# Optimization experiments

Measured on AMD Instinct MI355X. Metric: run time of the kernel, lower is better.

## Reference

```python
import jax, jax.numpy as jnp
import numpy as np

SIGMA = 1.2
SIGMA_SQ = jnp.float32(SIGMA * SIGMA)


def setup_inputs() -> dict:
    key = jax.random.key(0)
    k1, k2, k3 = jax.random.split(key, 3)
    X = jax.random.normal(k1, (32768, 2), dtype=jnp.float32)
    pattern_layer = jax.random.normal(k2, (8192, 2), dtype=jnp.float32)
    W2 = jax.random.normal(k3, (8192,), dtype=jnp.float32)
    return {"X": X, "pattern_layer": pattern_layer, "W2": W2}


def reference(X, pattern_layer, W2):
    # Pairwise squared distances via |a|^2 + |b|^2 - 2 a.b  -> [N, P]
    x_sq = jnp.sum(X * X, axis=1, keepdims=True)              # [N, 1]
    p_sq = jnp.sum(pattern_layer * pattern_layer, axis=1)     # [P]
    cross = X @ pattern_layer.T                               # [N, P]
    Dsq = x_sq + p_sq[None, :] - 2.0 * cross                  # [N, P]
    K = jnp.exp(-Dsq / (2.0 * SIGMA_SQ))                      # RBF kernel [N, P]
    num = K @ W2                                              # [N]
    den = jnp.sum(K, axis=1)                                  # [N]
    return num / den
```

## Files before the change

kernel.cpp:

```cpp
#include <hip/hip_runtime.h>

#define N 32768
#define P 8192
#define SLICES 8
#define XPB 64
#define PATS_PER_SLICE (P / SLICES)

#define RBF_F 0.50093577808645257f

static __device__ __forceinline__ float fast_exp2(float x) {
#if __has_builtin(__builtin_amdgcn_exp2f)
    return __builtin_amdgcn_exp2f(x);
#else
    return exp2f(x);
#endif
}

__global__ void prep_kernel(const float* __restrict__ pat,
                            const float* __restrict__ w2,
                            float4* __restrict__ c) {
    int i = blockIdx.x * blockDim.x + threadIdx.x;
    if (i < P) {
        float p0 = pat[2 * i];
        float p1 = pat[2 * i + 1];
        float4 v;
        v.x = 2.0f * RBF_F * p0;
        v.y = 2.0f * RBF_F * p1;
        v.z = -RBF_F * (p0 * p0 + p1 * p1);
        v.w = w2[i];
        c[i] = v;
    }
}

__global__ __launch_bounds__(SLICES * XPB) void
rbf_kernel(const float* __restrict__ X,
           const float4* __restrict__ c,
           float* __restrict__ out) {
    const int t  = threadIdx.x;
    const int xl = t & (XPB - 1);
    const int xi = blockIdx.x * XPB + xl;
    const int slice = __builtin_amdgcn_readfirstlane(t >> 6);

    const float2 xv = ((const float2*)X)[xi];
    const float x0 = xv.x, x1 = xv.y;

    const float4* __restrict__ cp = c + slice * PATS_PER_SLICE;

    float n0 = 0.f, n1 = 0.f, n2 = 0.f, n3 = 0.f;
    float d0 = 0.f, d1 = 0.f, d2 = 0.f, d3 = 0.f;

#pragma unroll 4
    for (int j = 0; j < PATS_PER_SLICE; j += 4) {
        float4 a = cp[j + 0];
        float4 b = cp[j + 1];
        float4 e = cp[j + 2];
        float4 g = cp[j + 3];

        float k0 = fast_exp2(fmaf(a.y, x1, fmaf(a.x, x0, a.z)));
        float k1 = fast_exp2(fmaf(b.y, x1, fmaf(b.x, x0, b.z)));
        float k2 = fast_exp2(fmaf(e.y, x1, fmaf(e.x, x0, e.z)));
        float k3 = fast_exp2(fmaf(g.y, x1, fmaf(g.x, x0, g.z)));

        d0 += k0; n0 = fmaf(k0, a.w, n0);
        d1 += k1; n1 = fmaf(k1, b.w, n1);
        d2 += k2; n2 = fmaf(k2, e.w, n2);
        d3 += k3; n3 = fmaf(k3, g.w, n3);
    }

    float num = (n0 + n1) + (n2 + n3);
    float den = (d0 + d1) + (d2 + d3);

    __shared__ float snum[SLICES][XPB];
    __shared__ float sden[SLICES][XPB];
    snum[slice][xl] = num;
    sden[slice][xl] = den;
    __syncthreads();

    if (t < XPB) {
        float nn = 0.f, dd = 0.f;
#pragma unroll
        for (int s = 0; s < SLICES; ++s) {
            nn += snum[s][t];
            dd += sden[s][t];
        }
        out[blockIdx.x * XPB + t] = nn / dd;
    }
}

extern "C" void kernel_launch(void* const* d_in, const int* in_sizes, int n_in,
                              void* d_out, int out_size, void* d_ws, size_t ws_size,
                              hipStream_t stream) {
    const float* X   = (const float*)d_in[0];
    const float* pat = (const float*)d_in[1];
    const float* w2  = (const float*)d_in[2];
    float* out = (float*)d_out;
    float4* c = (float4*)d_ws;

    prep_kernel<<<(P + 255) / 256, 256, 0, stream>>>(pat, w2, c);
    rbf_kernel<<<N / XPB, SLICES * XPB, 0, stream>>>(X, c, out);
}
```

Before: 109.2 us.

## Repack pattern constants into pair layout and use packed FP32 FMA

The prep kernel now stores patterns in pairs laid out structure-of-arrays within two float4s, so the main loop can evaluate two patterns at once with packed 2-wide FMA (v_pk_fma_f32) for both the exponent argument and the weighted accumulation. This cuts the VALU instruction count per pattern, leaving the transcendental exp2 as the main per-pattern cost. Slices per block double to 16 (1024 threads), which halves the per-thread loop length but doubles the shared-memory reduction and block size and may limit occupancy.

```diff
diff --git a/kernel.cpp b/kernel.cpp
--- a/kernel.cpp
+++ b/kernel.cpp
@@ -2,11 +2,14 @@
 
 #define N 32768
 #define P 8192
-#define SLICES 8
+#define SLICES 16
 #define XPB 64
 #define PATS_PER_SLICE (P / SLICES)
+#define PAIRS_PER_SLICE (PATS_PER_SLICE / 2)
 
 #define RBF_F 0.50093577808645257f
+
+typedef float v2f __attribute__((ext_vector_type(2)));
 
 static __device__ __forceinline__ float fast_exp2(float x) {
 #if __has_builtin(__builtin_amdgcn_exp2f)
@@ -19,16 +22,18 @@
 __global__ void prep_kernel(const float* __restrict__ pat,
                             const float* __restrict__ w2,
                             float4* __restrict__ c) {
-    int i = blockIdx.x * blockDim.x + threadIdx.x;
-    if (i < P) {
-        float p0 = pat[2 * i];
-        float p1 = pat[2 * i + 1];
-        float4 v;
-        v.x = 2.0f * RBF_F * p0;
-        v.y = 2.0f * RBF_F * p1;
-        v.z = -RBF_F * (p0 * p0 + p1 * p1);
-        v.w = w2[i];
-        c[i] = v;
+    int q = blockIdx.x * blockDim.x + threadIdx.x;
+    if (q < P / 2) {
+        float p00 = pat[4 * q + 0], p01 = pat[4 * q + 1];
+        float p10 = pat[4 * q + 2], p11 = pat[4 * q + 3];
+        float4 a, b;
+        a.x = 2.0f * RBF_F * p00;  a.y = 2.0f * RBF_F * p10;
+        a.z = 2.0f * RBF_F * p01;  a.w = 2.0f * RBF_F * p11;
+        b.x = -RBF_F * (p00 * p00 + p01 * p01);
+        b.y = -RBF_F * (p10 * p10 + p11 * p11);
+        b.z = w2[2 * q];           b.w = w2[2 * q + 1];
+        c[2 * q]     = a;
+        c[2 * q + 1] = b;
     }
 }
 
@@ -42,33 +47,41 @@
     const int slice = __builtin_amdgcn_readfirstlane(t >> 6);
 
     const float2 xv = ((const float2*)X)[xi];
-    const float x0 = xv.x, x1 = xv.y;
+    const v2f x0v = { xv.x, xv.x };
+    const v2f x1v = { xv.y, xv.y };
 
-    const float4* __restrict__ cp = c + slice * PATS_PER_SLICE;
+    const float4* __restrict__ cp = c + (size_t)slice * (2 * PAIRS_PER_SLICE);
 
-    float n0 = 0.f, n1 = 0.f, n2 = 0.f, n3 = 0.f;
-    float d0 = 0.f, d1 = 0.f, d2 = 0.f, d3 = 0.f;
+    v2f n0 = {0.f, 0.f}, n1 = {0.f, 0.f};
+    v2f d0 = {0.f, 0.f}, d1 = {0.f, 0.f};
 
-#pragma unroll 4
-    for (int j = 0; j < PATS_PER_SLICE; j += 4) {
-        float4 a = cp[j + 0];
-        float4 b = cp[j + 1];
-        float4 e = cp[j + 2];
-        float4 g = cp[j + 3];
+#pragma unroll 2
+    for (int q = 0; q < PAIRS_PER_SLICE; q += 2) {
+        float4 a0 = cp[2 * q + 0];
+        float4 a1 = cp[2 * q + 1];
+        float4 b0 = cp[2 * q + 2];
+        float4 b1 = cp[2 * q + 3];
 
-        float k0 = fast_exp2(fmaf(a.y, x1, fmaf(a.x, x0, a.z)));
-        float k1 = fast_exp2(fmaf(b.y, x1, fmaf(b.x, x0, b.z)));
-        float k2 = fast_exp2(fmaf(e.y, x1, fmaf(e.x, x0, e.z)));
-        float k3 = fast_exp2(fmaf(g.y, x1, fmaf(g.x, x0, g.z)));
+        v2f ta = __builtin_elementwise_fma((v2f){a0.x, a0.y}, x0v,
+                                           (v2f){a1.x, a1.y});
+        ta = __builtin_elementwise_fma((v2f){a0.z, a0.w}, x1v, ta);
+        v2f tb = __builtin_elementwise_fma((v2f){b0.x, b0.y}, x0v,
+                                           (v2f){b1.x, b1.y});
+        tb = __builtin_elementwise_fma((v2f){b0.z, b0.w}, x1v, tb);
 
-        d0 += k0; n0 = fmaf(k0, a.w, n0);
-        d1 += k1; n1 = fmaf(k1, b.w, n1);
-        d2 += k2; n2 = fmaf(k2, e.w, n2);
-        d3 += k3; n3 = fmaf(k3, g.w, n3);
+        v2f ka = { fast_exp2(ta.x), fast_exp2(ta.y) };
+        v2f kb = { fast_exp2(tb.x), fast_exp2(tb.y) };
+
+        d0 += ka;
+        n0 = __builtin_elementwise_fma(ka, (v2f){a1.z, a1.w}, n0);
+        d1 += kb;
+        n1 = __builtin_elementwise_fma(kb, (v2f){b1.z, b1.w}, n1);
     }
 
-    float num = (n0 + n1) + (n2 + n3);
-    float den = (d0 + d1) + (d2 + d3);
+    v2f nv = n0 + n1;
+    v2f dv = d0 + d1;
+    float num = nv.x + nv.y;
+    float den = dv.x + dv.y;
 
     __shared__ float snum[SLICES][XPB];
     __shared__ float sden[SLICES][XPB];
@@ -96,6 +109,6 @@
     float* out = (float*)d_out;
     float4* c = (float4*)d_ws;
 
-    prep_kernel<<<(P + 255) / 256, 256, 0, stream>>>(pat, w2, c);
+    prep_kernel<<<(P / 2 + 255) / 256, 256, 0, stream>>>(pat, w2, c);
     rbf_kernel<<<N / XPB, SLICES * XPB, 0, stream>>>(X, c, out);
 }
```

Result: faster. 99.15 us (-9.2%).

## Stage pattern tiles in LDS via async loads and use packed FMA over multiple points

Applied to the files above, without the earlier changes.

Swaps the mapping: each lane now handles a pattern and each wave covers 8 X points, where before each thread walked the patterns for a single point. Pattern tiles are double-buffered into LDS with global_load_lds, and the math uses packed v2f FMAs. Results are reduced with cross-lane shuffles and then shared memory. The intent is to cut per-thread global/L2 loads of the pattern constants and raise ALU throughput with packed ops, but exp2 throughput stays the bound. The change also adds a shuffle reduction and a sync per tile.

```diff
diff --git a/kernel.cpp b/kernel.cpp
--- a/kernel.cpp
+++ b/kernel.cpp
@@ -2,11 +2,20 @@
 
 #define N 32768
 #define P 8192
-#define SLICES 8
-#define XPB 64
-#define PATS_PER_SLICE (P / SLICES)
+#define TILE 1024
+#define NTILES (P / TILE)
+#define XG 4
+#define MX 8
+#define XPB (XG * MX)
+#define THREADS 512
+#define NBLK (N / XPB)
 
 #define RBF_F 0.50093577808645257f
+
+typedef float v2f __attribute__((ext_vector_type(2)));
+
+#define AS1 __attribute__((address_space(1)))
+#define AS3 __attribute__((address_space(3)))
 
 static __device__ __forceinline__ float fast_exp2(float x) {
 #if __has_builtin(__builtin_amdgcn_exp2f)
@@ -32,57 +41,97 @@
     }
 }
 
-__global__ __launch_bounds__(SLICES * XPB) void
+__global__ __launch_bounds__(THREADS, 8) void
 rbf_kernel(const float* __restrict__ X,
            const float4* __restrict__ c,
            float* __restrict__ out) {
-    const int t  = threadIdx.x;
-    const int xl = t & (XPB - 1);
-    const int xi = blockIdx.x * XPB + xl;
-    const int slice = __builtin_amdgcn_readfirstlane(t >> 6);
+    __shared__ float4 buf[2][TILE];
+    __shared__ float red[XG][2][MX][2];
 
-    const float2 xv = ((const float2*)X)[xi];
-    const float x0 = xv.x, x1 = xv.y;
+    const int t    = threadIdx.x;
+    const int lane = t & 63;
+    const int w    = __builtin_amdgcn_readfirstlane(t >> 6);
+    const int xg   = w >> 1;
+    const int ph   = w & 1;
 
-    const float4* __restrict__ cp = c + slice * PATS_PER_SLICE;
-
-    float n0 = 0.f, n1 = 0.f, n2 = 0.f, n3 = 0.f;
-    float d0 = 0.f, d1 = 0.f, d2 = 0.f, d3 = 0.f;
-
-#pragma unroll 4
-    for (int j = 0; j < PATS_PER_SLICE; j += 4) {
-        float4 a = cp[j + 0];
-        float4 b = cp[j + 1];
-        float4 e = cp[j + 2];
-        float4 g = cp[j + 3];
-
-        float k0 = fast_exp2(fmaf(a.y, x1, fmaf(a.x, x0, a.z)));
-        float k1 = fast_exp2(fmaf(b.y, x1, fmaf(b.x, x0, b.z)));
-        float k2 = fast_exp2(fmaf(e.y, x1, fmaf(e.x, x0, e.z)));
-        float k3 = fast_exp2(fmaf(g.y, x1, fmaf(g.x, x0, g.z)));
-
-        d0 += k0; n0 = fmaf(k0, a.w, n0);
-        d1 += k1; n1 = fmaf(k1, b.w, n1);
-        d2 += k2; n2 = fmaf(k2, e.w, n2);
-        d3 += k3; n3 = fmaf(k3, g.w, n3);
+    const int xbase = blockIdx.x * XPB + xg * MX;
+    v2f xs0[MX / 2], xs1[MX / 2];
+    {
+        const float2* Xp = (const float2*)X;
+#pragma unroll
+        for (int i = 0; i < MX / 2; ++i) {
+            float2 xa = Xp[xbase + 2 * i];
+            float2 xb = Xp[xbase + 2 * i + 1];
+            xs0[i] = (v2f){xa.x, xb.x};
+            xs1[i] = (v2f){xa.y, xb.y};
+        }
     }
 
-    float num = (n0 + n1) + (n2 + n3);
-    float den = (d0 + d1) + (d2 + d3);
+    v2f num[MX / 2], den[MX / 2];
+#pragma unroll
+    for (int i = 0; i < MX / 2; ++i) {
+        num[i] = (v2f){0.f, 0.f};
+        den[i] = (v2f){0.f, 0.f};
+    }
 
-    __shared__ float snum[SLICES][XPB];
-    __shared__ float sden[SLICES][XPB];
-    snum[slice][xl] = num;
-    sden[slice][xl] = den;
+    auto stage = [&](int tile, int bsel) {
+        const float4* src = c + tile * TILE;
+        __builtin_amdgcn_global_load_lds((const AS1 void*)(src + t),
+                                         (AS3 void*)&buf[bsel][t], 16, 0, 0);
+        __builtin_amdgcn_global_load_lds((const AS1 void*)(src + t + 512),
+                                         (AS3 void*)&buf[bsel][t + 512], 16, 0, 0);
+    };
+
+    stage(0, 0);
+    __syncthreads();
+
+    for (int tile = 0; tile < NTILES; ++tile) {
+        const int bsel = tile & 1;
+        if (tile + 1 < NTILES) stage(tile + 1, bsel ^ 1);
+
+        const float4* cur = &buf[bsel][ph * (TILE / 2)];
+#pragma unroll 2
+        for (int j = 0; j < TILE / 2; j += 64) {
+            float4 cc = cur[j + lane];
+#pragma unroll
+            for (int i = 0; i < MX / 2; ++i) {
+                v2f tt = __builtin_elementwise_fma((v2f){cc.x, cc.x}, xs0[i],
+                                                   (v2f){cc.z, cc.z});
+                tt = __builtin_elementwise_fma((v2f){cc.y, cc.y}, xs1[i], tt);
+                v2f k = (v2f){fast_exp2(tt.x), fast_exp2(tt.y)};
+                den[i] += k;
+                num[i] = __builtin_elementwise_fma(k, (v2f){cc.w, cc.w}, num[i]);
+            }
+        }
+        __syncthreads();
+    }
+
+#pragma unroll
+    for (int m = 1; m < 64; m <<= 1) {
+#pragma unroll
+        for (int i = 0; i < MX / 2; ++i) {
+            num[i].x += __shfl_xor(num[i].x, m, 64);
+            num[i].y += __shfl_xor(num[i].y, m, 64);
+            den[i].x += __shfl_xor(den[i].x, m, 64);
+            den[i].y += __shfl_xor(den[i].y, m, 64);
+        }
+    }
+
+    if (lane == 0) {
+#pragma unroll
+        for (int i = 0; i < MX / 2; ++i) {
+            red[xg][ph][2 * i][0]     = num[i].x;
+            red[xg][ph][2 * i][1]     = den[i].x;
+            red[xg][ph][2 * i + 1][0] = num[i].y;
+            red[xg][ph][2 * i + 1][1] = den[i].y;
+        }
+    }
     __syncthreads();
 
     if (t < XPB) {
-        float nn = 0.f, dd = 0.f;
-#pragma unroll
-        for (int s = 0; s < SLICES; ++s) {
-            nn += snum[s][t];
-            dd += sden[s][t];
-        }
+        int g = t >> 3, xi = t & 7;
+        float nn = red[g][0][xi][0] + red[g][1][xi][0];
+        float dd = red[g][0][xi][1] + red[g][1][xi][1];
         out[blockIdx.x * XPB + t] = nn / dd;
     }
 }
@@ -97,5 +146,5 @@
     float4* c = (float4*)d_ws;
 
     prep_kernel<<<(P + 255) / 256, 256, 0, stream>>>(pat, w2, c);
-    rbf_kernel<<<N / XPB, SLICES * XPB, 0, stream>>>(X, c, out);
+    rbf_kernel<<<NBLK, THREADS, 0, stream>>>(X, c, out);
 }
```

Measured after the change: 96.25 us. 1.13x faster.

## Compute RBF exponents in packed fp16 and reduce num/den with MFMA

Applied to the files above, without the earlier changes.

Switches exponent evaluation to packed half2 FMA and h2exp2, two patterns per instruction. The weighted sum and the denominator move onto a 16x16x32 f16 MFMA, with the B matrix holding W2 in one column and ones in another. The work is regrouped into 16-point tiles split across 4 waves, and the next chunk is prefetched in registers. This halves exp/FMA issue and offloads the accumulation, but fp16 exponents and kernel values lose precision and may underflow, which risks accuracy.

```diff
diff --git a/kernel.cpp b/kernel.cpp
--- a/kernel.cpp
+++ b/kernel.cpp
@@ -1,89 +1,122 @@
 #include <hip/hip_runtime.h>
+#include <hip/hip_fp16.h>
 
 #define N 32768
 #define P 8192
-#define SLICES 8
-#define XPB 64
-#define PATS_PER_SLICE (P / SLICES)
+#define XT 16
+#define WAVES 4
+#define THREADS (WAVES * 64)
+#define NBLK (N / XT)
+#define CHUNK 32
+#define CPW (P / WAVES / CHUNK)
 
 #define RBF_F 0.50093577808645257f
 
-static __device__ __forceinline__ float fast_exp2(float x) {
-#if __has_builtin(__builtin_amdgcn_exp2f)
-    return __builtin_amdgcn_exp2f(x);
-#else
-    return exp2f(x);
-#endif
-}
+typedef _Float16 h2  __attribute__((ext_vector_type(2)));
+typedef _Float16 v8h __attribute__((ext_vector_type(8)));
+typedef float    v4f __attribute__((ext_vector_type(4)));
 
 __global__ void prep_kernel(const float* __restrict__ pat,
                             const float* __restrict__ w2,
-                            float4* __restrict__ c) {
-    int i = blockIdx.x * blockDim.x + threadIdx.x;
-    if (i < P) {
-        float p0 = pat[2 * i];
-        float p1 = pat[2 * i + 1];
-        float4 v;
-        v.x = 2.0f * RBF_F * p0;
-        v.y = 2.0f * RBF_F * p1;
-        v.z = -RBF_F * (p0 * p0 + p1 * p1);
-        v.w = w2[i];
-        c[i] = v;
+                            _Float16* __restrict__ QA,
+                            _Float16* __restrict__ WH) {
+    int q = blockIdx.x * blockDim.x + threadIdx.x;
+    if (q < P / 2) {
+        float p00 = pat[4 * q + 0], p01 = pat[4 * q + 1];
+        float p10 = pat[4 * q + 2], p11 = pat[4 * q + 3];
+        v8h r;
+        r[0] = (_Float16)(2.0f * RBF_F * p00);
+        r[1] = (_Float16)(2.0f * RBF_F * p10);
+        r[2] = (_Float16)(2.0f * RBF_F * p01);
+        r[3] = (_Float16)(2.0f * RBF_F * p11);
+        r[4] = (_Float16)(-RBF_F * (p00 * p00 + p01 * p01));
+        r[5] = (_Float16)(-RBF_F * (p10 * p10 + p11 * p11));
+        r[6] = (_Float16)0.0f;
+        r[7] = (_Float16)0.0f;
+        ((v8h*)QA)[q] = r;
+        WH[2 * q]     = (_Float16)w2[2 * q];
+        WH[2 * q + 1] = (_Float16)w2[2 * q + 1];
     }
 }
 
-__global__ __launch_bounds__(SLICES * XPB) void
+__global__ __launch_bounds__(THREADS) void
 rbf_kernel(const float* __restrict__ X,
-           const float4* __restrict__ c,
+           const _Float16* __restrict__ QA,
+           const _Float16* __restrict__ WH,
            float* __restrict__ out) {
-    const int t  = threadIdx.x;
-    const int xl = t & (XPB - 1);
-    const int xi = blockIdx.x * XPB + xl;
-    const int slice = __builtin_amdgcn_readfirstlane(t >> 6);
+    const int t    = threadIdx.x;
+    const int lane = t & 63;
+    const int wv   = __builtin_amdgcn_readfirstlane(t >> 6);
+    const int n16  = lane & 15;
+    const int quad = lane >> 4;
 
-    const float2 xv = ((const float2*)X)[xi];
-    const float x0 = xv.x, x1 = xv.y;
+    const float2 xv = ((const float2*)X)[blockIdx.x * XT + n16];
+    const __half2 xx0 = __float2half2_rn(xv.x);
+    const __half2 xx1 = __float2half2_rn(xv.y);
 
-    const float4* __restrict__ cp = c + slice * PATS_PER_SLICE;
+    v8h btpl;
+#pragma unroll
+    for (int j = 0; j < 8; ++j)
+        btpl[j] = (n16 == 1) ? (_Float16)1.0f : (_Float16)0.0f;
 
-    float n0 = 0.f, n1 = 0.f, n2 = 0.f, n3 = 0.f;
-    float d0 = 0.f, d1 = 0.f, d2 = 0.f, d3 = 0.f;
+    v4f acc = {0.f, 0.f, 0.f, 0.f};
 
-#pragma unroll 4
-    for (int j = 0; j < PATS_PER_SLICE; j += 4) {
-        float4 a = cp[j + 0];
-        float4 b = cp[j + 1];
-        float4 e = cp[j + 2];
-        float4 g = cp[j + 3];
+    const v8h* __restrict__ QA8 = (const v8h*)QA;
+    const int pb = (wv * CPW) * 16 + quad * 4;
+    const _Float16* __restrict__ WB = WH + (wv * CPW) * 32 + quad * 8;
 
-        float k0 = fast_exp2(fmaf(a.y, x1, fmaf(a.x, x0, a.z)));
-        float k1 = fast_exp2(fmaf(b.y, x1, fmaf(b.x, x0, b.z)));
-        float k2 = fast_exp2(fmaf(e.y, x1, fmaf(e.x, x0, e.z)));
-        float k3 = fast_exp2(fmaf(g.y, x1, fmaf(g.x, x0, g.z)));
+    auto cell2 = [&](v8h q) -> __half2 {
+        __half2 c0 = __builtin_bit_cast(__half2, (h2)__builtin_shufflevector(q, q, 0, 1));
+        __half2 c1 = __builtin_bit_cast(__half2, (h2)__builtin_shufflevector(q, q, 2, 3));
+        __half2 c2 = __builtin_bit_cast(__half2, (h2)__builtin_shufflevector(q, q, 4, 5));
+        __half2 tt = __hfma2(c0, xx0, __hfma2(c1, xx1, c2));
+        return h2exp2(tt);
+    };
 
-        d0 += k0; n0 = fmaf(k0, a.w, n0);
-        d1 += k1; n1 = fmaf(k1, b.w, n1);
-        d2 += k2; n2 = fmaf(k2, e.w, n2);
-        d3 += k3; n3 = fmaf(k3, g.w, n3);
+    v8h qc0 = QA8[pb + 0], qc1 = QA8[pb + 1], qc2 = QA8[pb + 2], qc3 = QA8[pb + 3];
+    v8h bc = btpl;
+    if (n16 == 0) bc = *(const v8h*)WB;
+
+#pragma unroll 2
+    for (int ch = 0; ch < CPW; ++ch) {
+        const int chn = (ch + 1) & (CPW - 1);
+        v8h qn0 = QA8[pb + chn * 16 + 0];
+        v8h qn1 = QA8[pb + chn * 16 + 1];
+        v8h qn2 = QA8[pb + chn * 16 + 2];
+        v8h qn3 = QA8[pb + chn * 16 + 3];
+        v8h bn = btpl;
+        if (n16 == 0) bn = *(const v8h*)(WB + chn * 32);
+
+        __half2 k0 = cell2(qc0), k1 = cell2(qc1), k2 = cell2(qc2), k3 = cell2(qc3);
+        h2 k0h = __builtin_bit_cast(h2, k0);
+        h2 k1h = __builtin_bit_cast(h2, k1);
+        h2 k2h = __builtin_bit_cast(h2, k2);
+        h2 k3h = __builtin_bit_cast(h2, k3);
+        v8h a;
+        a[0] = k0h.x; a[1] = k0h.y; a[2] = k1h.x; a[3] = k1h.y;
+        a[4] = k2h.x; a[5] = k2h.y; a[6] = k3h.x; a[7] = k3h.y;
+
+        acc = __builtin_amdgcn_mfma_f32_16x16x32_f16(a, bc, acc, 0, 0, 0);
+
+        qc0 = qn0; qc1 = qn1; qc2 = qn2; qc3 = qn3; bc = bn;
     }
 
-    float num = (n0 + n1) + (n2 + n3);
-    float den = (d0 + d1) + (d2 + d3);
-
-    __shared__ float snum[SLICES][XPB];
-    __shared__ float sden[SLICES][XPB];
-    snum[slice][xl] = num;
-    sden[slice][xl] = den;
+    __shared__ float red[WAVES][XT][2];
+    if (n16 < 2) {
+#pragma unroll
+        for (int r = 0; r < 4; ++r)
+            red[wv][quad * 4 + r][n16] = acc[r];
+    }
     __syncthreads();
 
-    if (t < XPB) {
+    if (t < XT) {
         float nn = 0.f, dd = 0.f;
 #pragma unroll
-        for (int s = 0; s < SLICES; ++s) {
-            nn += snum[s][t];
-            dd += sden[s][t];
+        for (int w = 0; w < WAVES; ++w) {
+            nn += red[w][t][0];
+            dd += red[w][t][1];
         }
-        out[blockIdx.x * XPB + t] = nn / dd;
+        out[blockIdx.x * XT + t] = nn / dd;
     }
 }
 
@@ -94,8 +127,10 @@
     const float* pat = (const float*)d_in[1];
     const float* w2  = (const float*)d_in[2];
     float* out = (float*)d_out;
-    float4* c = (float4*)d_ws;
 
-    prep_kernel<<<(P + 255) / 256, 256, 0, stream>>>(pat, w2, c);
-    rbf_kernel<<<N / XPB, SLICES * XPB, 0, stream>>>(X, c, out);
+    _Float16* QA = (_Float16*)d_ws;
+    _Float16* WH = QA + (size_t)P * 4;
+
+    prep_kernel<<<(P / 2 + 255) / 256, 256, 0, stream>>>(pat, w2, QA, WH);
+    rbf_kernel<<<NBLK, THREADS, 0, stream>>>(X, QA, WH, out);
 }
```

Result: slower. 131.1 us (+20.0%).
